# Kernel optimization log

Measured on AMD Instinct MI355X. Metric: run time of the kernel, lower is better.

## Reference

```python
import jax, jax.numpy as jnp
import numpy as np

BOX = 5  # box_size (odd)
PATTERN_SCALE = 16.0


def setup_inputs() -> dict:
    key = jax.random.key(0)
    k1, k2 = jax.random.split(key)
    x = jax.random.normal(k1, (1, 1, 480, 640), dtype=jnp.float32)
    # buffer: uniform in [-pattern_scale, pattern_scale], shape [num_pairs, 2, 2]
    pair_offsets = (jax.random.uniform(k2, (256, 2, 2), dtype=jnp.float32) - 0.5) * 2.0 * PATTERN_SCALE
    return {"x": x, "pair_offsets": pair_offsets}


def _box_average(x, box):
    # replicate-pad then stride-1 average pool => same-size box average
    pad = box // 2
    xp = jnp.pad(x, ((0, 0), (0, 0), (pad, pad), (pad, pad)), mode='edge')
    s = jax.lax.reduce_window(xp, 0.0, jax.lax.add,
                              (1, 1, box, box), (1, 1, 1, 1), 'VALID')
    return s / float(box * box)


def _grid_sample_offsets(img_flat, offsets, B, H, W):
    """Bilinear grid_sample with border padding, align_corners=True,
    for per-pair translational grids. img_flat: [B, H*W]; offsets: [P, 2] (dy, dx).
    Returns [B, P, H, W]."""
    scale_y = 2.0 / (H - 1 + 1e-8)
    scale_x = 2.0 / (W - 1 + 1e-8)
    base_y = jnp.linspace(-1.0, 1.0, H, dtype=img_flat.dtype)[None, :, None]  # [1,H,1]
    base_x = jnp.linspace(-1.0, 1.0, W, dtype=img_flat.dtype)[None, None, :]  # [1,1,W]
    gy = base_y + offsets[:, 0, None, None] * scale_y  # [P,H,1]
    gx = base_x + offsets[:, 1, None, None] * scale_x  # [P,1,W]
    # unnormalize (align_corners=True) and clip coords (padding_mode='border')
    py = jnp.clip((gy + 1.0) * 0.5 * (H - 1), 0.0, H - 1.0)  # [P,H,1]
    px = jnp.clip((gx + 1.0) * 0.5 * (W - 1), 0.0, W - 1.0)  # [P,1,W]
    y0 = jnp.floor(py)
    x0 = jnp.floor(px)
    wy = py - y0  # [P,H,1]
    wx = px - x0  # [P,1,W]
    y0i = y0.astype(jnp.int32)
    x0i = x0.astype(jnp.int32)
    y1i = jnp.minimum(y0i + 1, H - 1)
    x1i = jnp.minimum(x0i + 1, W - 1)

    def gather(yi, xi):
        idx = yi * W + xi  # broadcast -> [P,H,W]
        return jnp.take(img_flat, idx, axis=1)  # [B,P,H,W]

    v = (gather(y0i, x0i) * (1.0 - wy) * (1.0 - wx)
         + gather(y0i, x1i) * (1.0 - wy) * wx
         + gather(y1i, x0i) * wy * (1.0 - wx)
         + gather(y1i, x1i) * wy * wx)
    return v


def reference(x, pair_offsets):
    B, C, H, W = x.shape
    box_avg = _box_average(x, BOX)            # [B,1,H,W]
    img_flat = box_avg[:, 0].reshape(B, H * W)
    s1 = _grid_sample_offsets(img_flat, pair_offsets[:, 0, :], B, H, W)
    s2 = _grid_sample_offsets(img_flat, pair_offsets[:, 1, :], B, H, W)
    return s1 - s2  # binarize=False -> raw differences, [B, P, H, W]
```

## Files before the change

### kernel.cpp

```cpp
#include <hip/hip_runtime.h>

#define H 480
#define W 640
#define NP 256
#define HW (H * W)

#define P1_BLK 16
#define P2_BLK 9
#define P3_BLK 14
#define P4_BLK 8

#define P1_TOTAL (NP * P1_BLK)
#define P2_TOTAL (NP * (P1_BLK + P2_BLK))
#define P3_TOTAL (NP * (P1_BLK + P2_BLK + P3_BLK))
#define TOTAL_BLK (NP * (P1_BLK + P2_BLK + P3_BLK + P4_BLK))

typedef float f32x4 __attribute__((ext_vector_type(4)));

__device__ __forceinline__ void nt_store4(float* p, float a, float b, float c, float d) {
    f32x4 v = {a, b, c, d};
    __builtin_nontemporal_store(v, (f32x4*)p);
}

__global__ __launch_bounds__(256) void box_avg_kernel(const float* __restrict__ x,
                                                      float* __restrict__ box) {
    int idx = blockIdx.x * 256 + threadIdx.x;
    int i = idx / W;
    int j = idx - i * W;
    float s = 0.f;
#pragma unroll
    for (int dy = -2; dy <= 2; ++dy) {
        int yy = min(max(i + dy, 0), H - 1);
        const float* row = x + yy * W;
#pragma unroll
        for (int dx = -2; dx <= 2; ++dx) {
            int xx = min(max(j + dx, 0), W - 1);
            s += row[xx];
        }
    }
    box[idx] = s * 0.04f;
}

template<int S>
__device__ __forceinline__ void hlerp8(const float4 P, const float4 Q, const float4 R,
                                       float wx, float h[8]) {
    const float c[12] = {P.x, P.y, P.z, P.w, Q.x, Q.y, Q.z, Q.w, R.x, R.y, R.z, R.w};
#pragma unroll
    for (int k = 0; k < 8; ++k)
        h[k] = fmaf(wx, c[S + k + 1] - c[S + k], c[S + k]);
}

#define DISPATCH_H(sv, ...)                              \
    switch (sv) {                                        \
        case 0:  hlerp8<0>(__VA_ARGS__); break;          \
        case 1:  hlerp8<1>(__VA_ARGS__); break;          \
        case 2:  hlerp8<2>(__VA_ARGS__); break;          \
        default: hlerp8<3>(__VA_ARGS__); break;          \
    }

__global__ __launch_bounds__(256) void bad_desc_kernel(const float* __restrict__ box,
                                                       const float* __restrict__ po,
                                                       float* __restrict__ out) {
    int b = blockIdx.x;
    if (b < P1_TOTAL) {
        int p = b >> 4;
        int t = ((b - (p << 4)) << 8) + threadIdx.x;
        int band = t / 72;
        if (band >= 56) return;
        int g = t - band * 72;
        int i0 = 16 + (band << 3);
        int j  = 32 + (g << 3);

        float dy1 = po[p * 4 + 0];
        float dx1 = po[p * 4 + 1];
        float dy2 = po[p * 4 + 2];
        float dx2 = po[p * 4 + 3];

        float fj = (float)j;

        float xf1 = fj + dx1;
        float fl1 = floorf(xf1);
        int   x01 = (int)fl1;
        float wx1 = xf1 - fl1;
        int   s1  = __builtin_amdgcn_readfirstlane(x01 & 3);
        int   m1  = min(max(x01 - (x01 & 3), 0), W - 12);

        float xf2 = fj + dx2;
        float fl2 = floorf(xf2);
        int   x02 = (int)fl2;
        float wx2 = xf2 - fl2;
        int   s2  = __builtin_amdgcn_readfirstlane(x02 & 3);
        int   m2  = min(max(x02 - (x02 & 3), 0), W - 12);

        float fdy1 = floorf(dy1);
        float wy1  = dy1 - fdy1;
        int   rA   = min(max(i0 + (int)fdy1, 0), H - 9);
        float fdy2 = floorf(dy2);
        float wy2  = dy2 - fdy2;
        int   rB   = min(max(i0 + (int)fdy2, 0), H - 9);

        const float* baseA = box + rA * W + m1;
        const float* baseB = box + rB * W + m2;

        float h1p[8], h2p[8], h1c[8], h2c[8];
        {
            const float4* ra = (const float4*)baseA;
            const float4* rb = (const float4*)baseB;
            float4 Pa = ra[0], Qa = ra[1], Ra = ra[2];
            float4 Pb = rb[0], Qb = rb[1], Rb = rb[2];
            DISPATCH_H(s1, Pa, Qa, Ra, wx1, h1p);
            DISPATCH_H(s2, Pb, Qb, Rb, wx2, h2p);
        }

        float* o = out + ((size_t)p * HW + (size_t)i0 * W + (size_t)j);
        for (int k = 1; k <= 8; ++k) {
            const float4* ra = (const float4*)(baseA + k * W);
            const float4* rb = (const float4*)(baseB + k * W);
            float4 Pa = ra[0], Qa = ra[1], Ra = ra[2];
            float4 Pb = rb[0], Qb = rb[1], Rb = rb[2];
            DISPATCH_H(s1, Pa, Qa, Ra, wx1, h1c);
            DISPATCH_H(s2, Pb, Qb, Rb, wx2, h2c);

            float v[8];
#pragma unroll
            for (int q = 0; q < 8; ++q) {
                float a = fmaf(wy1, h1c[q] - h1p[q], h1p[q]);
                float c = fmaf(wy2, h2c[q] - h2p[q], h2p[q]);
                v[q] = a - c;
                h1p[q] = h1c[q];
                h2p[q] = h2c[q];
            }
            nt_store4(o,     v[0], v[1], v[2], v[3]);
            nt_store4(o + 4, v[4], v[5], v[6], v[7]);
            o += W;
        }
    } else if (b < P2_TOTAL) {
        int b2 = b - P1_TOTAL;
        int p = b2 / P2_BLK;
        int t = (b2 - p * P2_BLK) * 256 + threadIdx.x;
        int ii = t / 72;
        int g  = t - ii * 72;
        int i  = (ii < 16) ? ii : 448 + ii;
        int j  = 32 + (g << 3);

        float dy1 = po[p * 4 + 0];
        float dx1 = po[p * 4 + 1];
        float dy2 = po[p * 4 + 2];
        float dx2 = po[p * 4 + 3];

        float fi = (float)i;
        float fj = (float)j;

        float py1 = fminf(fmaxf(fi + dy1, 0.f), (float)(H - 1));
        int   ya0 = (int)py1;
        float wy1 = py1 - (float)ya0;
        int   ya1 = min(ya0 + 1, H - 1);

        float xf1 = fj + dx1;
        float fl1 = floorf(xf1);
        int   x01 = (int)fl1;
        float wx1 = xf1 - fl1;
        int   s1  = __builtin_amdgcn_readfirstlane(x01 & 3);
        int   m1  = min(max(x01 - (x01 & 3), 0), W - 12);

        const float4* r1a = (const float4*)(box + ya0 * W + m1);
        const float4* r1b = (const float4*)(box + ya1 * W + m1);
        float4 Pa = r1a[0], Qa = r1a[1], Ra = r1a[2];
        float4 Pb = r1b[0], Qb = r1b[1], Rb = r1b[2];
        float ha[8], hb[8];
        DISPATCH_H(s1, Pa, Qa, Ra, wx1, ha);
        DISPATCH_H(s1, Pb, Qb, Rb, wx1, hb);

        float py2 = fminf(fmaxf(fi + dy2, 0.f), (float)(H - 1));
        int   yb0 = (int)py2;
        float wy2 = py2 - (float)yb0;
        int   yb1 = min(yb0 + 1, H - 1);

        float xf2 = fj + dx2;
        float fl2 = floorf(xf2);
        int   x02 = (int)fl2;
        float wx2 = xf2 - fl2;
        int   s2  = __builtin_amdgcn_readfirstlane(x02 & 3);
        int   m2  = min(max(x02 - (x02 & 3), 0), W - 12);

        const float4* r2a = (const float4*)(box + yb0 * W + m2);
        const float4* r2b = (const float4*)(box + yb1 * W + m2);
        float4 Pc = r2a[0], Qc = r2a[1], Rc = r2a[2];
        float4 Pd = r2b[0], Qd = r2b[1], Rd = r2b[2];
        float hc[8], hd[8];
        DISPATCH_H(s2, Pc, Qc, Rc, wx2, hc);
        DISPATCH_H(s2, Pd, Qd, Rd, wx2, hd);

        float v[8];
#pragma unroll
        for (int q = 0; q < 8; ++q) {
            float a = fmaf(wy1, hb[q] - ha[q], ha[q]);
            float c = fmaf(wy2, hd[q] - hc[q], hc[q]);
            v[q] = a - c;
        }
        float* o = out + ((size_t)p * HW + (size_t)i * W + (size_t)j);
        nt_store4(o,     v[0], v[1], v[2], v[3]);
        nt_store4(o + 4, v[4], v[5], v[6], v[7]);
    } else if (b < P3_TOTAL) {
        int b2 = b - P2_TOTAL;
        int p = b2 / P3_BLK;
        int t = (b2 - p * P3_BLK) * 256 + threadIdx.x;
        int band = t >> 6;
        int c = t & 63;
        int i0 = 16 + (band << 3);
        int j  = (c < 32) ? c : 576 + c;

        float dy1 = po[p * 4 + 0];
        float dx1 = po[p * 4 + 1];
        float dy2 = po[p * 4 + 2];
        float dx2 = po[p * 4 + 3];

        float fj = (float)j;

        float px1 = fminf(fmaxf(fj + dx1, 0.f), (float)(W - 1));
        int   xa0 = (int)px1;
        float wxa = px1 - (float)xa0;
        int   xa1 = min(xa0 + 1, W - 1);

        float px2 = fminf(fmaxf(fj + dx2, 0.f), (float)(W - 1));
        int   xb0 = (int)px2;
        float wxb = px2 - (float)xb0;
        int   xb1 = min(xb0 + 1, W - 1);

        float fdy1 = floorf(dy1);
        float wy1  = dy1 - fdy1;
        int   rA   = min(max(i0 + (int)fdy1, 0), H - 9);
        float fdy2 = floorf(dy2);
        float wy2  = dy2 - fdy2;
        int   rB   = min(max(i0 + (int)fdy2, 0), H - 9);

        const float* pA = box + rA * W;
        const float* pB = box + rB * W;

        float a0 = pA[xa0], a1 = pA[xa1];
        float h1p = fmaf(wxa, a1 - a0, a0);
        float b0 = pB[xb0], b1 = pB[xb1];
        float h2p = fmaf(wxb, b1 - b0, b0);

        float* o = out + ((size_t)p * HW + (size_t)i0 * W + (size_t)j);
        for (int k = 1; k <= 8; ++k) {
            const float* qA = pA + k * W;
            const float* qB = pB + k * W;
            float c0 = qA[xa0], c1 = qA[xa1];
            float h1c = fmaf(wxa, c1 - c0, c0);
            float d0 = qB[xb0], d1 = qB[xb1];
            float h2c = fmaf(wxb, d1 - d0, d0);

            float va = fmaf(wy1, h1c - h1p, h1p);
            float vb = fmaf(wy2, h2c - h2p, h2p);
            __builtin_nontemporal_store(va - vb, o);
            h1p = h1c;
            h2p = h2c;
            o += W;
        }
    } else {
        int b2 = b - P3_TOTAL;
        int p = b2 >> 3;
        int t = ((b2 - (p << 3)) << 8) + threadIdx.x;
        int ii = t >> 6;
        int c = t & 63;
        int i = (ii < 16) ? ii : 448 + ii;
        int j = (c < 32) ? c : 576 + c;

        float dy1 = po[p * 4 + 0];
        float dx1 = po[p * 4 + 1];
        float dy2 = po[p * 4 + 2];
        float dx2 = po[p * 4 + 3];

        float fi = (float)i;
        float fj = (float)j;

        float py1 = fminf(fmaxf(fi + dy1, 0.f), (float)(H - 1));
        int   ya0 = (int)py1;
        float wy1 = py1 - (float)ya0;
        int   ya1 = min(ya0 + 1, H - 1);
        const float* r1a = box + ya0 * W;
        const float* r1b = box + ya1 * W;

        float px = fminf(fmaxf(fj + dx1, 0.f), (float)(W - 1));
        int   x0 = (int)px;
        float wx = px - (float)x0;
        int   x1 = min(x0 + 1, W - 1);
        float a0 = r1a[x0], a1 = r1a[x1];
        float b0 = r1b[x0], b1 = r1b[x1];
        float h0 = fmaf(wx, a1 - a0, a0);
        float h1 = fmaf(wx, b1 - b0, b0);
        float v1 = fmaf(wy1, h1 - h0, h0);

        float py2 = fminf(fmaxf(fi + dy2, 0.f), (float)(H - 1));
        int   yb0 = (int)py2;
        float wy2 = py2 - (float)yb0;
        int   yb1 = min(yb0 + 1, H - 1);
        const float* r2a = box + yb0 * W;
        const float* r2b = box + yb1 * W;

        float qx = fminf(fmaxf(fj + dx2, 0.f), (float)(W - 1));
        int   u0 = (int)qx;
        float ux = qx - (float)u0;
        int   u1 = min(u0 + 1, W - 1);
        float c0 = r2a[u0], c1 = r2a[u1];
        float d0 = r2b[u0], d1 = r2b[u1];
        float g0 = fmaf(ux, c1 - c0, c0);
        float g1 = fmaf(ux, d1 - d0, d0);
        float v2 = fmaf(wy2, g1 - g0, g0);

        __builtin_nontemporal_store(v1 - v2, out + ((size_t)p * HW + (size_t)i * W + (size_t)j));
    }
}

extern "C" void kernel_launch(void* const* d_in, const int* in_sizes, int n_in,
                              void* d_out, int out_size, void* d_ws, size_t ws_size,
                              hipStream_t stream) {
    const float* x  = (const float*)d_in[0];
    const float* po = (const float*)d_in[1];
    float* out = (float*)d_out;
    float* box = (float*)d_ws;

    box_avg_kernel<<<HW / 256, 256, 0, stream>>>(x, box);
    bad_desc_kernel<<<TOTAL_BLK, 256, 0, stream>>>(box, po, out);
}
```

Baseline: 331.5 us.

## Repartition interior/border regions to 64-wide waves and shuffle for coalesced row stores

Each wavefront in the interior region now covers 64 eight-pixel groups, spanning 512 columns of one row. Before storing, lanes exchange values through cross-lane shuffles so that each store instruction writes a fully contiguous 1 KB span instead of strided 32-byte pieces. The interior/border split shifts from 32 to 64 border columns, and the block counts per region are rebalanced to match. This is meant to improve write coalescing on the store-bound output, at the cost of extra shuffle instructions and more work sent to the slower per-pixel border paths.

```diff
diff --git a/kernel.cpp b/kernel.cpp
--- a/kernel.cpp
+++ b/kernel.cpp
@@ -5,10 +5,10 @@
 #define NP 256
 #define HW (H * W)
 
-#define P1_BLK 16
-#define P2_BLK 9
-#define P3_BLK 14
-#define P4_BLK 8
+#define P1_BLK 14
+#define P2_BLK 8
+#define P3_BLK 28
+#define P4_BLK 16
 
 #define P1_TOTAL (NP * P1_BLK)
 #define P2_TOTAL (NP * (P1_BLK + P2_BLK))
@@ -63,13 +63,12 @@
                                                        float* __restrict__ out) {
     int b = blockIdx.x;
     if (b < P1_TOTAL) {
-        int p = b >> 4;
-        int t = ((b - (p << 4)) << 8) + threadIdx.x;
-        int band = t / 72;
-        if (band >= 56) return;
-        int g = t - band * 72;
+        int p = b / P1_BLK;
+        int t = (b - p * P1_BLK) * 256 + threadIdx.x;
+        int band = t >> 6;
+        int g = t & 63;
         int i0 = 16 + (band << 3);
-        int j  = 32 + (g << 3);
+        int j  = 64 + (g << 3);
 
         float dy1 = po[p * 4 + 0];
         float dx1 = po[p * 4 + 1];
@@ -112,7 +111,12 @@
             DISPATCH_H(s2, Pb, Qb, Rb, wx2, h2p);
         }
 
-        float* o = out + ((size_t)p * HW + (size_t)i0 * W + (size_t)j);
+        int lane = g;
+        int sA = lane >> 1;
+        int sB = sA + 32;
+        int odd = lane & 1;
+        float* rowo = out + ((size_t)p * HW + (size_t)i0 * W + 64);
+
         for (int k = 1; k <= 8; ++k) {
             const float4* ra = (const float4*)(baseA + k * W);
             const float4* rb = (const float4*)(baseB + k * W);
@@ -130,18 +134,28 @@
                 h1p[q] = h1c[q];
                 h2p[q] = h2c[q];
             }
-            nt_store4(o,     v[0], v[1], v[2], v[3]);
-            nt_store4(o + 4, v[4], v[5], v[6], v[7]);
-            o += W;
+            float A[4], Bv[4];
+#pragma unroll
+            for (int d = 0; d < 4; ++d) {
+                float p0 = __shfl(v[d],     sA, 64);
+                float p1 = __shfl(v[d + 4], sA, 64);
+                A[d] = odd ? p1 : p0;
+                float q0 = __shfl(v[d],     sB, 64);
+                float q1 = __shfl(v[d + 4], sB, 64);
+                Bv[d] = odd ? q1 : q0;
+            }
+            float* ro = rowo + (size_t)(k - 1) * W;
+            nt_store4(ro + (lane << 2),        A[0],  A[1],  A[2],  A[3]);
+            nt_store4(ro + 256 + (lane << 2),  Bv[0], Bv[1], Bv[2], Bv[3]);
         }
     } else if (b < P2_TOTAL) {
         int b2 = b - P1_TOTAL;
         int p = b2 / P2_BLK;
         int t = (b2 - p * P2_BLK) * 256 + threadIdx.x;
-        int ii = t / 72;
-        int g  = t - ii * 72;
+        int ii = t >> 6;
+        int g  = t & 63;
         int i  = (ii < 16) ? ii : 448 + ii;
-        int j  = 32 + (g << 3);
+        int j  = 64 + (g << 3);
 
         float dy1 = po[p * 4 + 0];
         float dx1 = po[p * 4 + 1];
@@ -205,10 +219,10 @@
         int b2 = b - P2_TOTAL;
         int p = b2 / P3_BLK;
         int t = (b2 - p * P3_BLK) * 256 + threadIdx.x;
-        int band = t >> 6;
-        int c = t & 63;
+        int band = t >> 7;
+        int c = t & 127;
         int i0 = 16 + (band << 3);
-        int j  = (c < 32) ? c : 576 + c;
+        int j  = (c < 64) ? c : 512 + c;
 
         float dy1 = po[p * 4 + 0];
         float dx1 = po[p * 4 + 1];
@@ -260,12 +274,12 @@
         }
     } else {
         int b2 = b - P3_TOTAL;
-        int p = b2 >> 3;
-        int t = ((b2 - (p << 3)) << 8) + threadIdx.x;
-        int ii = t >> 6;
-        int c = t & 63;
+        int p = b2 / P4_BLK;
+        int t = (b2 - p * P4_BLK) * 256 + threadIdx.x;
+        int ii = t >> 7;
+        int c = t & 127;
         int i = (ii < 16) ? ii : 448 + ii;
-        int j = (c < 32) ? c : 576 + c;
+        int j = (c < 64) ? c : 512 + c;
 
         float dy1 = po[p * 4 + 0];
         float dx1 = po[p * 4 + 1];
```

Measured after the change: 320.8 us. -3.2%, faster.
